# Kernel optimization log

Hardware: AMD Instinct MI355X
Metric: run time of the kernel (lower is better)

## Reference

```python
import jax, jax.numpy as jnp
import numpy as np

# MX microscaling decode helpers. Codes are stored as int32 holding uint8 bit patterns.
_FP4_MAG = jnp.array([0.0, 0.5, 1.0, 1.5, 2.0, 3.0, 4.0, 6.0], dtype=jnp.float32)  # E2M1

def dec_fp4(c):
    # c in [0,16): bit3 = sign, bits0-2 index E2M1 magnitude LUT
    s = jnp.where(c >= 8, -1.0, 1.0)
    return s * _FP4_MAG[c & 7]

def dec_fp6(c):
    # E3M2, bias 3. bit5 sign, bits2-4 exp, bits0-1 mantissa
    s = jnp.where(c >= 32, -1.0, 1.0)
    e = ((c >> 2) & 7).astype(jnp.float32)
    m = (c & 3).astype(jnp.float32)
    mag = jnp.where(e == 0, m * 0.25 * 0.25, (1.0 + m * 0.25) * jnp.exp2(e - 3.0))
    return s * mag

def dec_fp8(c):
    # E4M3, bias 7. bit7 sign, bits3-6 exp, bits0-2 mantissa (NaN code decoded as 480, consistent both sides)
    s = jnp.where(c >= 128, -1.0, 1.0)
    e = ((c >> 3) & 15).astype(jnp.float32)
    m = (c & 7).astype(jnp.float32)
    mag = jnp.where(e == 0, m * 0.125 * jnp.exp2(-6.0), (1.0 + m * 0.125) * jnp.exp2(e - 7.0))
    return s * mag

def unpack4(p):
    # [..., K//2] bytes -> [..., K] nibbles; low nibble = even element, high = odd
    lo = p & 15
    hi = (p >> 4) & 15
    return jnp.stack([lo, hi], axis=-1).reshape(*p.shape[:-1], p.shape[-1] * 2)

def unpack6(p):
    # little-endian 6-bit packing: 4 values per 3 bytes. [..., K*6//8] -> [..., K]
    g = p.reshape(*p.shape[:-1], -1, 3)
    b0, b1, b2 = g[..., 0], g[..., 1], g[..., 2]
    v0 = b0 & 0x3F
    v1 = ((b0 >> 6) & 3) | ((b1 & 0x0F) << 2)
    v2 = ((b1 >> 4) & 0x0F) | ((b2 & 3) << 4)
    v3 = (b2 >> 2) & 0x3F
    return jnp.stack([v0, v1, v2, v3], axis=-1).reshape(*p.shape[:-1], p.shape[-1] * 4 // 3)

def blockscale(x, sf):
    # x [..., K] fp32, sf [..., K//32] E8M0 exponents: scale = 2^(sf-127) per 32-element block
    scale = jnp.exp2(sf.astype(jnp.float32) - 127.0)
    xs = x.reshape(*x.shape[:-1], -1, 32) * scale[..., None]
    return xs.reshape(x.shape)

def dequant(codes, sf, bits):
    if bits == 4:
        x = dec_fp4(unpack4(codes))
    elif bits == 6:
        x = dec_fp6(unpack6(codes))
    else:
        x = dec_fp8(codes)
    return blockscale(x, sf)


def setup_inputs() -> dict:
    key = jax.random.key(0)
    ks = jax.random.split(key, 13)
    M, N = 4096, 4096
    p4, p6, p8 = 3072, 768, 256
    ri = lambda k, sh: jax.random.randint(k, sh, 0, 256, dtype=jnp.int32)
    sf = lambda k, sh: jax.random.randint(k, sh, 121, 132, dtype=jnp.int32)
    return {
        "AN": ri(ks[0], (M, p4 // 2)),
        "AS": ri(ks[1], (M, p6 * 6 // 8)),
        "AO": ri(ks[2], (M, p8)),
        "SFAN": sf(ks[3], (M, p4 // 32)),
        "SFAS": sf(ks[4], (M, p6 // 32)),
        "SFAO": sf(ks[5], (M, p8 // 32)),
        "BN": ri(ks[6], (N, p4 // 2)),
        "BS": ri(ks[7], (N, p6 * 6 // 8)),
        "BO": ri(ks[8], (N, p8)),
        "SFBN": sf(ks[9], (N * p4 // 32,)),
        "SFBS": sf(ks[10], (N * p6 // 32,)),
        "SFBO": sf(ks[11], (N * p8 // 32,)),
        "bias": jax.random.normal(ks[12], (N,), dtype=jnp.float32) * 0.02,
    }


def reference(AN, AS, AO, SFAN, SFAS, SFAO, BN, BS, BO, SFBN, SFBS, SFBO, bias):
    N = BN.shape[0]
    a4 = dequant(AN, SFAN, 4)                       # [M, p4]
    w4 = dequant(BN, SFBN.reshape(N, -1), 4)        # [N, p4]
    a6 = dequant(AS, SFAS, 6)                       # [M, p6]
    w6 = dequant(BS, SFBS.reshape(N, -1), 6)        # [N, p6]
    a8 = dequant(AO, SFAO, 8)                       # [M, p8]
    w8 = dequant(BO, SFBO.reshape(N, -1), 8)        # [N, p8]
    y = a4 @ w4.T + a6 @ w6.T + a8 @ w8.T           # [M, N]
    return y + bias
```

## Files before the change

kernel.cpp:

```cpp
#include <hip/hip_runtime.h>

typedef short short8 __attribute__((ext_vector_type(8)));
typedef int   intx8  __attribute__((ext_vector_type(8)));
typedef float floatx16 __attribute__((ext_vector_type(16)));

__device__ __forceinline__ unsigned pk4(int a, int b, int c, int d) {
    return (a & 255) | ((b & 255) << 8) | ((c & 255) << 16) | ((unsigned)(d & 255) << 24);
}

__device__ __forceinline__ unsigned dec8bf(int c, int esf) {
    int s = (c & 128) << 8;
    int e = (c >> 3) & 15, m = c & 7;
    int rn = s | ((e + 120 + esf) << 7) | (m << 4);
    int nb = (m >= 4) ? 2 : ((m >= 2) ? 1 : 0);
    int rs = m ? (s | ((nb + 118 + esf) << 7) | ((m << (7 - nb)) & 0x7F)) : s;
    return (unsigned)(e ? rn : rs);
}

__global__ __launch_bounds__(256) void pack_lds(
    const int* __restrict__ Pn, const int* __restrict__ Ps, const int* __restrict__ Po,
    const int* __restrict__ Sn, const int* __restrict__ Ss, const int* __restrict__ So,
    unsigned char* __restrict__ C4, unsigned char* __restrict__ C6,
    unsigned short* __restrict__ C8, unsigned char* __restrict__ St, int R)
{
    __shared__ unsigned lds[9216];
    int t = threadIdx.x, b = blockIdx.x, per = R >> 6;
    if (b < 4 * per) {
        int jg = b / per, rb = b - jg * per, r0 = rb << 6;
        #pragma unroll
        for (int i = 0; i < 24; ++i) {
            int idx = i * 256 + t, row = idx / 96, q4 = idx - row * 96;
            int4 v = *(const int4*)(Pn + (size_t)(r0 + row) * 1536 + jg * 384 + q4 * 4);
            lds[row * 96 + q4] = pk4(v.x, v.y, v.z, v.w);
        }
        __syncthreads();
        #pragma unroll
        for (int i = 0; i < 6; ++i) {
            int idx = i * 256 + t, j = idx >> 6, row = idx & 63;
            uint4 v = *(uint4*)&lds[row * 96 + j * 4];
            *(uint4*)(C4 + ((size_t)(jg * 24 + j) * R + r0 + row) * 16) = v;
        }
    } else if (b < 5 * per) {
        int rb = b - 4 * per, r0 = rb << 6;
        #pragma unroll
        for (int i = 0; i < 36; ++i) {
            int idx = i * 256 + t, row = idx / 144, q4 = idx - row * 144;
            int4 v = *(const int4*)(Ps + (size_t)(r0 + row) * 576 + q4 * 4);
            lds[row * 144 + q4] = pk4(v.x, v.y, v.z, v.w);
        }
        __syncthreads();
        #pragma unroll
        for (int i = 0; i < 18; ++i) {
            int idx = i * 256 + t, seg = idx / 192, off = idx - seg * 192;
            int row = off / 3, m3 = off - row * 3;
            int w0 = row * 144 + seg * 6 + m3 * 2;
            int2 v = { (int)lds[w0], (int)lds[w0 + 1] };
            *(int2*)(C6 + ((size_t)seg * R + r0) * 24 + (size_t)off * 8) = v;
        }
    } else if (b < 6 * per) {
        int rb = b - 5 * per, r0 = rb << 6;
        #pragma unroll
        for (int i = 0; i < 16; ++i) {
            int idx = i * 256 + t, row = idx >> 6, q4 = idx & 63;
            int4 c = *(const int4*)(Po + (size_t)(r0 + row) * 256 + q4 * 4);
            int e = So[(size_t)(r0 + row) * 8 + (q4 >> 3)] - 127;
            lds[row * 128 + q4 * 2]     = dec8bf(c.x & 255, e) | (dec8bf(c.y & 255, e) << 16);
            lds[row * 128 + q4 * 2 + 1] = dec8bf(c.z & 255, e) | (dec8bf(c.w & 255, e) << 16);
        }
        __syncthreads();
        #pragma unroll
        for (int i = 0; i < 8; ++i) {
            int idx = i * 256 + t, seg = idx >> 6, row = idx & 63;
            uint4 v = *(uint4*)&lds[row * 128 + seg * 4];
            *(uint4*)((unsigned char*)C8 + ((size_t)seg * R + r0 + row) * 16) = v;
        }
    } else if (b < 7 * per) {
        int rb = b - 6 * per, r0 = rb << 6;
        #pragma unroll
        for (int i = 0; i < 6; ++i) {
            int idx = i * 256 + t, row = idx / 24, q4 = idx - row * 24;
            int4 v = *(const int4*)(Sn + (size_t)(r0 + row) * 96 + q4 * 4);
            lds[row * 24 + q4] = pk4(v.x, v.y, v.z, v.w);
        }
        __syncthreads();
        #pragma unroll
        for (int i = 0; i < 6; ++i) {
            int idx = i * 256 + t, seg = idx >> 6, row = idx & 63;
            *(unsigned*)(St + ((size_t)seg * R + r0 + row) * 4) = lds[row * 24 + seg];
        }
    } else {
        int rb = b - 7 * per, r0 = rb << 6;
        #pragma unroll
        for (int i = 0; i < 3; ++i) {
            int idx = i * 256 + t, row = idx / 12, b2 = idx - row * 12;
            int2 v = *(const int2*)(Ss + (size_t)(r0 + row) * 24 + b2 * 2);
            lds[row * 12 + b2] = (unsigned)((v.x & 255) | ((v.y & 255) << 8));
        }
        __syncthreads();
        #pragma unroll
        for (int i = 0; i < 3; ++i) {
            int idx = i * 256 + t, seg = idx >> 6, row = idx & 63;
            *(unsigned*)(St + ((size_t)(24 + seg) * R + r0 + row) * 4) = lds[row * 12 + seg];
        }
    }
}

__global__ __launch_bounds__(256, 2) void gemm_mx(
    const unsigned char* __restrict__ A4, const unsigned char* __restrict__ B4,
    const unsigned char* __restrict__ A6, const unsigned char* __restrict__ B6,
    const unsigned short* __restrict__ A8, const unsigned short* __restrict__ B8,
    const unsigned char* __restrict__ SaT, const unsigned char* __restrict__ SbT,
    const float* __restrict__ bias, float* __restrict__ C, int M, int N)
{
    int tid = threadIdx.x, w = tid >> 6, l = tid & 63;
    int nbm = M >> 7, nbn = N >> 7;
    int bm, bn;
    if (nbm == 32 && nbn == 32) {
        int o = blockIdx.y * 32 + blockIdx.x;
        int xcd = o & 7, pos = o >> 3;
        int tile = pos >> 4, idx = pos & 15;
        bm = xcd * 4 + (idx & 3);
        bn = tile * 4 + (idx >> 2);
    } else { bm = blockIdx.y; bn = blockIdx.x; }

    int wm = (w >> 1) * 64, wn = (w & 1) * 64;
    int lr = l & 31, lh = l >> 5;

    floatx16 acc[2][2] = {};

    int rA[2] = { bm * 128 + wm + lr, bm * 128 + wm + 32 + lr };
    int cB[2] = { bn * 128 + wn + lr, bn * 128 + wn + 32 + lr };

    {
        unsigned strA = 32u * (unsigned)M, strB = 32u * (unsigned)N;
        unsigned fA0 = ((unsigned)lh * M + (unsigned)rA[0]) * 16u;
        unsigned fA1 = ((unsigned)lh * M + (unsigned)rA[1]) * 16u;
        unsigned fB0 = ((unsigned)lh * N + (unsigned)cB[0]) * 16u;
        unsigned fB1 = ((unsigned)lh * N + (unsigned)cB[1]) * 16u;

        int4 pa[4][2], pb[4][2];
        #pragma unroll
        for (int s = 0; s < 4; ++s) {
            pa[s][0] = *(const int4*)(A4 + fA0); pa[s][1] = *(const int4*)(A4 + fA1);
            pb[s][0] = *(const int4*)(B4 + fB0); pb[s][1] = *(const int4*)(B4 + fB1);
            fA0 += strA; fA1 += strA; fB0 += strB; fB1 += strB;
        }

        unsigned sstrA = 4u * (unsigned)M, sstrB = 4u * (unsigned)N;
        unsigned sA0 = (unsigned)rA[0] * 4u, sA1 = (unsigned)rA[1] * 4u;
        unsigned sB0 = (unsigned)cB[0] * 4u, sB1 = (unsigned)cB[1] * 4u;
        unsigned psa[2][2], psb[2][2];
        psa[0][0] = *(const unsigned*)(SaT + sA0);         psa[0][1] = *(const unsigned*)(SaT + sA1);
        psb[0][0] = *(const unsigned*)(SbT + sB0);         psb[0][1] = *(const unsigned*)(SbT + sB1);
        psa[1][0] = *(const unsigned*)(SaT + sA0 + sstrA); psa[1][1] = *(const unsigned*)(SaT + sA1 + sstrA);
        psb[1][0] = *(const unsigned*)(SbT + sB0 + sstrB); psb[1][1] = *(const unsigned*)(SbT + sB1 + sstrB);
        sA0 += 2 * sstrA; sA1 += 2 * sstrA; sB0 += 2 * sstrB; sB1 += 2 * sstrB;

        #pragma unroll 4
        for (int u = 0; u < 48; ++u) {
            int sl = u & 3, wsl = (u >> 1) & 1;
            int sh = 8 * ((u & 1) * 2 + lh);
            int sa0 = (int)((psa[wsl][0] >> sh) & 255), sa1 = (int)((psa[wsl][1] >> sh) & 255);
            int sb0 = (int)((psb[wsl][0] >> sh) & 255), sb1 = (int)((psb[wsl][1] >> sh) & 255);
            intx8 A0 = (intx8){ pa[sl][0].x, pa[sl][0].y, pa[sl][0].z, pa[sl][0].w, 0, 0, 0, 0 };
            intx8 A1 = (intx8){ pa[sl][1].x, pa[sl][1].y, pa[sl][1].z, pa[sl][1].w, 0, 0, 0, 0 };
            intx8 B0 = (intx8){ pb[sl][0].x, pb[sl][0].y, pb[sl][0].z, pb[sl][0].w, 0, 0, 0, 0 };
            intx8 B1 = (intx8){ pb[sl][1].x, pb[sl][1].y, pb[sl][1].z, pb[sl][1].w, 0, 0, 0, 0 };
            acc[0][0] = __builtin_amdgcn_mfma_scale_f32_32x32x64_f8f6f4(A0, B0, acc[0][0], 4, 4, 0, sa0, 0, sb0);
            acc[0][1] = __builtin_amdgcn_mfma_scale_f32_32x32x64_f8f6f4(A0, B1, acc[0][1], 4, 4, 0, sa0, 0, sb1);
            acc[1][0] = __builtin_amdgcn_mfma_scale_f32_32x32x64_f8f6f4(A1, B0, acc[1][0], 4, 4, 0, sa1, 0, sb0);
            acc[1][1] = __builtin_amdgcn_mfma_scale_f32_32x32x64_f8f6f4(A1, B1, acc[1][1], 4, 4, 0, sa1, 0, sb1);
            pa[sl][0] = *(const int4*)(A4 + fA0); pa[sl][1] = *(const int4*)(A4 + fA1);
            pb[sl][0] = *(const int4*)(B4 + fB0); pb[sl][1] = *(const int4*)(B4 + fB1);
            fA0 += strA; fA1 += strA; fB0 += strB; fB1 += strB;
            if (u & 1) {
                psa[wsl][0] = *(const unsigned*)(SaT + sA0); psa[wsl][1] = *(const unsigned*)(SaT + sA1);
                psb[wsl][0] = *(const unsigned*)(SbT + sB0); psb[wsl][1] = *(const unsigned*)(SbT + sB1);
                sA0 += sstrA; sA1 += sstrA; sB0 += sstrB; sB1 += sstrB;
            }
        }
    }

    {
        unsigned str6A = 48u * (unsigned)M, str6B = 48u * (unsigned)N;
        unsigned gA0 = ((unsigned)lh * M + (unsigned)rA[0]) * 24u;
        unsigned gA1 = ((unsigned)lh * M + (unsigned)rA[1]) * 24u;
        unsigned gB0 = ((unsigned)lh * N + (unsigned)cB[0]) * 24u;
        unsigned gB1 = ((unsigned)lh * N + (unsigned)cB[1]) * 24u;
        unsigned ss4A = 4u * (unsigned)M, ss4B = 4u * (unsigned)N;
        unsigned zA0 = (24u * (unsigned)M + (unsigned)rA[0]) * 4u;
        unsigned zA1 = (24u * (unsigned)M + (unsigned)rA[1]) * 4u;
        unsigned zB0 = (24u * (unsigned)N + (unsigned)cB[0]) * 4u;
        unsigned zB1 = (24u * (unsigned)N + (unsigned)cB[1]) * 4u;

        int2 qa[2][2][3], qb[2][2][3];
        unsigned p6a[2][2], p6b[2][2];
        #pragma unroll
        for (int s = 0; s < 2; ++s) {
            const unsigned char *a0 = A6 + gA0, *a1 = A6 + gA1, *b0 = B6 + gB0, *b1 = B6 + gB1;
            qa[s][0][0] = *(const int2*)(a0); qa[s][0][1] = *(const int2*)(a0 + 8); qa[s][0][2] = *(const int2*)(a0 + 16);
            qa[s][1][0] = *(const int2*)(a1); qa[s][1][1] = *(const int2*)(a1 + 8); qa[s][1][2] = *(const int2*)(a1 + 16);
            qb[s][0][0] = *(const int2*)(b0); qb[s][0][1] = *(const int2*)(b0 + 8); qb[s][0][2] = *(const int2*)(b0 + 16);
            qb[s][1][0] = *(const int2*)(b1); qb[s][1][1] = *(const int2*)(b1 + 8); qb[s][1][2] = *(const int2*)(b1 + 16);
            p6a[s][0] = *(const unsigned*)(SaT + zA0); p6a[s][1] = *(const unsigned*)(SaT + zA1);
            p6b[s][0] = *(const unsigned*)(SbT + zB0); p6b[s][1] = *(const unsigned*)(SbT + zB1);
            gA0 += str6A; gA1 += str6A; gB0 += str6B; gB1 += str6B;
            zA0 += ss4A; zA1 += ss4A; zB0 += ss4B; zB1 += ss4B;
        }
        int sh6 = 8 * lh;
        #pragma unroll 2
        for (int v = 0; v < 10; ++v) {
            int sl = v & 1;
            int sa0 = (int)((p6a[sl][0] >> sh6) & 255), sa1 = (int)((p6a[sl][1] >> sh6) & 255);
            int sb0 = (int)((p6b[sl][0] >> sh6) & 255), sb1 = (int)((p6b[sl][1] >> sh6) & 255);
            intx8 A0 = (intx8){ qa[sl][0][0].x, qa[sl][0][0].y, qa[sl][0][1].x, qa[sl][0][1].y, qa[sl][0][2].x, qa[sl][0][2].y, 0, 0 };
            intx8 A1 = (intx8){ qa[sl][1][0].x, qa[sl][1][0].y, qa[sl][1][1].x, qa[sl][1][1].y, qa[sl][1][2].x, qa[sl][1][2].y, 0, 0 };
            intx8 B0 = (intx8){ qb[sl][0][0].x, qb[sl][0][0].y, qb[sl][0][1].x, qb[sl][0][1].y, qb[sl][0][2].x, qb[sl][0][2].y, 0, 0 };
            intx8 B1 = (intx8){ qb[sl][1][0].x, qb[sl][1][0].y, qb[sl][1][1].x, qb[sl][1][1].y, qb[sl][1][2].x, qb[sl][1][2].y, 0, 0 };
            acc[0][0] = __builtin_amdgcn_mfma_scale_f32_32x32x64_f8f6f4(A0, B0, acc[0][0], 3, 3, 0, sa0, 0, sb0);
            acc[0][1] = __builtin_amdgcn_mfma_scale_f32_32x32x64_f8f6f4(A0, B1, acc[0][1], 3, 3, 0, sa0, 0, sb1);
            acc[1][0] = __builtin_amdgcn_mfma_scale_f32_32x32x64_f8f6f4(A1, B0, acc[1][0], 3, 3, 0, sa1, 0, sb0);
            acc[1][1] = __builtin_amdgcn_mfma_scale_f32_32x32x64_f8f6f4(A1, B1, acc[1][1], 3, 3, 0, sa1, 0, sb1);
            {
                const unsigned char *a0 = A6 + gA0, *a1 = A6 + gA1, *b0 = B6 + gB0, *b1 = B6 + gB1;
                qa[sl][0][0] = *(const int2*)(a0); qa[sl][0][1] = *(const int2*)(a0 + 8); qa[sl][0][2] = *(const int2*)(a0 + 16);
                qa[sl][1][0] = *(const int2*)(a1); qa[sl][1][1] = *(const int2*)(a1 + 8); qa[sl][1][2] = *(const int2*)(a1 + 16);
                qb[sl][0][0] = *(const int2*)(b0); qb[sl][0][1] = *(const int2*)(b0 + 8); qb[sl][0][2] = *(const int2*)(b0 + 16);
                qb[sl][1][0] = *(const int2*)(b1); qb[sl][1][1] = *(const int2*)(b1 + 8); qb[sl][1][2] = *(const int2*)(b1 + 16);
                p6a[sl][0] = *(const unsigned*)(SaT + zA0); p6a[sl][1] = *(const unsigned*)(SaT + zA1);
                p6b[sl][0] = *(const unsigned*)(SbT + zB0); p6b[sl][1] = *(const unsigned*)(SbT + zB1);
                gA0 += str6A; gA1 += str6A; gB0 += str6B; gB1 += str6B;
                zA0 += ss4A; zA1 += ss4A; zB0 += ss4B; zB1 += ss4B;
            }
        }
        #pragma unroll
        for (int v = 10; v < 12; ++v) {
            int sl = v & 1;
            int sa0 = (int)((p6a[sl][0] >> sh6) & 255), sa1 = (int)((p6a[sl][1] >> sh6) & 255);
            int sb0 = (int)((p6b[sl][0] >> sh6) & 255), sb1 = (int)((p6b[sl][1] >> sh6) & 255);
            intx8 A0 = (intx8){ qa[sl][0][0].x, qa[sl][0][0].y, qa[sl][0][1].x, qa[sl][0][1].y, qa[sl][0][2].x, qa[sl][0][2].y, 0, 0 };
            intx8 A1 = (intx8){ qa[sl][1][0].x, qa[sl][1][0].y, qa[sl][1][1].x, qa[sl][1][1].y, qa[sl][1][2].x, qa[sl][1][2].y, 0, 0 };
            intx8 B0 = (intx8){ qb[sl][0][0].x, qb[sl][0][0].y, qb[sl][0][1].x, qb[sl][0][1].y, qb[sl][0][2].x, qb[sl][0][2].y, 0, 0 };
            intx8 B1 = (intx8){ qb[sl][1][0].x, qb[sl][1][0].y, qb[sl][1][1].x, qb[sl][1][1].y, qb[sl][1][2].x, qb[sl][1][2].y, 0, 0 };
            acc[0][0] = __builtin_amdgcn_mfma_scale_f32_32x32x64_f8f6f4(A0, B0, acc[0][0], 3, 3, 0, sa0, 0, sb0);
            acc[0][1] = __builtin_amdgcn_mfma_scale_f32_32x32x64_f8f6f4(A0, B1, acc[0][1], 3, 3, 0, sa0, 0, sb1);
            acc[1][0] = __builtin_amdgcn_mfma_scale_f32_32x32x64_f8f6f4(A1, B0, acc[1][0], 3, 3, 0, sa1, 0, sb0);
            acc[1][1] = __builtin_amdgcn_mfma_scale_f32_32x32x64_f8f6f4(A1, B1, acc[1][1], 3, 3, 0, sa1, 0, sb1);
        }
    }

    {
        unsigned str8A = 32u * (unsigned)M, str8B = 32u * (unsigned)N;
        const unsigned char* A8b = (const unsigned char*)A8;
        const unsigned char* B8b = (const unsigned char*)B8;
        unsigned hA0 = ((unsigned)lh * M + (unsigned)rA[0]) * 16u;
        unsigned hA1 = ((unsigned)lh * M + (unsigned)rA[1]) * 16u;
        unsigned hB0 = ((unsigned)lh * N + (unsigned)cB[0]) * 16u;
        unsigned hB1 = ((unsigned)lh * N + (unsigned)cB[1]) * 16u;
        short8 ra[2][2], rb[2][2];
        #pragma unroll
        for (int s = 0; s < 2; ++s) {
            ra[s][0] = *(const short8*)(A8b + hA0); ra[s][1] = *(const short8*)(A8b + hA1);
            rb[s][0] = *(const short8*)(B8b + hB0); rb[s][1] = *(const short8*)(B8b + hB1);
            hA0 += str8A; hA1 += str8A; hB0 += str8B; hB1 += str8B;
        }
        #pragma unroll 2
        for (int q = 0; q < 16; ++q) {
            int sl = q & 1;
            acc[0][0] = __builtin_amdgcn_mfma_f32_32x32x16_bf16(ra[sl][0], rb[sl][0], acc[0][0], 0, 0, 0);
            acc[0][1] = __builtin_amdgcn_mfma_f32_32x32x16_bf16(ra[sl][0], rb[sl][1], acc[0][1], 0, 0, 0);
            acc[1][0] = __builtin_amdgcn_mfma_f32_32x32x16_bf16(ra[sl][1], rb[sl][0], acc[1][0], 0, 0, 0);
            acc[1][1] = __builtin_amdgcn_mfma_f32_32x32x16_bf16(ra[sl][1], rb[sl][1], acc[1][1], 0, 0, 0);
            ra[sl][0] = *(const short8*)(A8b + hA0); ra[sl][1] = *(const short8*)(A8b + hA1);
            rb[sl][0] = *(const short8*)(B8b + hB0); rb[sl][1] = *(const short8*)(B8b + hB1);
            hA0 += str8A; hA1 += str8A; hB0 += str8B; hB1 += str8B;
        }
    }

    #pragma unroll
    for (int i = 0; i < 2; i++)
        #pragma unroll
        for (int j = 0; j < 2; j++) {
            int col = bn * 128 + wn + j * 32 + lr;
            float bv = bias[col];
            #pragma unroll
            for (int r = 0; r < 16; r++) {
                int row = bm * 128 + wm + i * 32 + (r & 3) + 8 * (r >> 2) + 4 * lh;
                C[(size_t)row * N + col] = acc[i][j][r] + bv;
            }
        }
}

extern "C" void kernel_launch(void* const* d_in, const int* in_sizes, int n_in,
                              void* d_out, int out_size, void* d_ws, size_t ws_size,
                              hipStream_t stream) {
    const int* AN   = (const int*)d_in[0];
    const int* ASs  = (const int*)d_in[1];
    const int* AO   = (const int*)d_in[2];
    const int* SFAN = (const int*)d_in[3];
    const int* SFAS = (const int*)d_in[4];
    const int* SFAO = (const int*)d_in[5];
    const int* BN   = (const int*)d_in[6];
    const int* BS   = (const int*)d_in[7];
    const int* BO   = (const int*)d_in[8];
    const int* SFBN = (const int*)d_in[9];
    const int* SFBS = (const int*)d_in[10];
    const int* SFBO = (const int*)d_in[11];
    const float* bias = (const float*)d_in[12];

    int M = in_sizes[0] / 1536;
    int N = in_sizes[6] / 1536;

    unsigned char* ws = (unsigned char*)d_ws;
    size_t o = 0;
    unsigned char*  A4c = ws + o;                    o += (size_t)M * 1536;
    unsigned char*  B4c = ws + o;                    o += (size_t)N * 1536;
    unsigned char*  A6c = ws + o;                    o += (size_t)M * 576;
    unsigned char*  B6c = ws + o;                    o += (size_t)N * 576;
    unsigned short* A8d = (unsigned short*)(ws + o); o += (size_t)M * 512;
    unsigned short* B8d = (unsigned short*)(ws + o); o += (size_t)N * 512;
    unsigned char*  SaT = ws + o;                    o += (size_t)36 * M * 4;
    unsigned char*  SbT = ws + o;                    o += (size_t)36 * N * 4;

    pack_lds<<<(M >> 6) * 8, 256, 0, stream>>>(AN, ASs, AO, SFAN, SFAS, SFAO,
                                               A4c, A6c, A8d, SaT, M);
    pack_lds<<<(N >> 6) * 8, 256, 0, stream>>>(BN, BS, BO, SFBN, SFBS, SFBO,
                                               B4c, B6c, B8d, SbT, N);

    dim3 grid(N / 128, M / 128);
    gemm_mx<<<grid, 256, 0, stream>>>(A4c, B4c, A6c, B6c, A8d, B8d,
                                      SaT, SbT, bias, (float*)d_out, M, N);
}
```

Measured before the change: 220.1 us.

## Merge A/B pack launches, drop XCD swizzle, reorder loads before prioritized MFMAs

Merges the two pack launches into one kernel whose grid covers both A and B sides, saving a launch and letting the two halves overlap. In the GEMM main loops, the next-stage global loads are now issued before the MFMAs, and each MFMA group is wrapped in s_setprio raises to favour matrix issue. The XCD-aware block-to-tile remap is removed in favour of a plain blockIdx mapping, which may reduce L2 locality across XCDs.

```diff
diff --git a/kernel.cpp b/kernel.cpp
--- a/kernel.cpp
+++ b/kernel.cpp
@@ -17,14 +17,14 @@
     return (unsigned)(e ? rn : rs);
 }
 
-__global__ __launch_bounds__(256) void pack_lds(
+__device__ __forceinline__ void pack_side_lds(
+    int b, int t, unsigned* lds,
     const int* __restrict__ Pn, const int* __restrict__ Ps, const int* __restrict__ Po,
     const int* __restrict__ Sn, const int* __restrict__ Ss, const int* __restrict__ So,
     unsigned char* __restrict__ C4, unsigned char* __restrict__ C6,
     unsigned short* __restrict__ C8, unsigned char* __restrict__ St, int R)
 {
-    __shared__ unsigned lds[9216];
-    int t = threadIdx.x, b = blockIdx.x, per = R >> 6;
+    int per = R >> 6;
     if (b < 4 * per) {
         int jg = b / per, rb = b - jg * per, r0 = rb << 6;
         #pragma unroll
@@ -103,6 +103,23 @@
             *(unsigned*)(St + ((size_t)(24 + seg) * R + r0 + row) * 4) = lds[row * 12 + seg];
         }
     }
+}
+
+__global__ __launch_bounds__(256) void pack_all(
+    const int* __restrict__ AN, const int* __restrict__ AS, const int* __restrict__ AO,
+    const int* __restrict__ SAn, const int* __restrict__ SAs, const int* __restrict__ SAo,
+    unsigned char* __restrict__ A4, unsigned char* __restrict__ A6,
+    unsigned short* __restrict__ A8, unsigned char* __restrict__ SaT, int M,
+    const int* __restrict__ BN, const int* __restrict__ BS, const int* __restrict__ BO,
+    const int* __restrict__ SBn, const int* __restrict__ SBs, const int* __restrict__ SBo,
+    unsigned char* __restrict__ B4, unsigned char* __restrict__ B6,
+    unsigned short* __restrict__ B8, unsigned char* __restrict__ SbT, int N)
+{
+    __shared__ unsigned lds[9216];
+    int b = blockIdx.x, t = threadIdx.x;
+    int nA = (M >> 6) * 8;
+    if (b < nA) pack_side_lds(b, t, lds, AN, AS, AO, SAn, SAs, SAo, A4, A6, A8, SaT, M);
+    else        pack_side_lds(b - nA, t, lds, BN, BS, BO, SBn, SBs, SBo, B4, B6, B8, SbT, N);
 }
 
 __global__ __launch_bounds__(256, 2) void gemm_mx(
@@ -113,16 +130,7 @@
     const float* __restrict__ bias, float* __restrict__ C, int M, int N)
 {
     int tid = threadIdx.x, w = tid >> 6, l = tid & 63;
-    int nbm = M >> 7, nbn = N >> 7;
-    int bm, bn;
-    if (nbm == 32 && nbn == 32) {
-        int o = blockIdx.y * 32 + blockIdx.x;
-        int xcd = o & 7, pos = o >> 3;
-        int tile = pos >> 4, idx = pos & 15;
-        bm = xcd * 4 + (idx & 3);
-        bn = tile * 4 + (idx >> 2);
-    } else { bm = blockIdx.y; bn = blockIdx.x; }
-
+    int bm = blockIdx.y, bn = blockIdx.x;
     int wm = (w >> 1) * 64, wn = (w & 1) * 64;
     int lr = l & 31, lh = l >> 5;
 
@@ -159,17 +167,13 @@
         #pragma unroll 4
         for (int u = 0; u < 48; ++u) {
             int sl = u & 3, wsl = (u >> 1) & 1;
-            int sh = 8 * ((u & 1) * 2 + lh);
-            int sa0 = (int)((psa[wsl][0] >> sh) & 255), sa1 = (int)((psa[wsl][1] >> sh) & 255);
-            int sb0 = (int)((psb[wsl][0] >> sh) & 255), sb1 = (int)((psb[wsl][1] >> sh) & 255);
             intx8 A0 = (intx8){ pa[sl][0].x, pa[sl][0].y, pa[sl][0].z, pa[sl][0].w, 0, 0, 0, 0 };
             intx8 A1 = (intx8){ pa[sl][1].x, pa[sl][1].y, pa[sl][1].z, pa[sl][1].w, 0, 0, 0, 0 };
             intx8 B0 = (intx8){ pb[sl][0].x, pb[sl][0].y, pb[sl][0].z, pb[sl][0].w, 0, 0, 0, 0 };
             intx8 B1 = (intx8){ pb[sl][1].x, pb[sl][1].y, pb[sl][1].z, pb[sl][1].w, 0, 0, 0, 0 };
-            acc[0][0] = __builtin_amdgcn_mfma_scale_f32_32x32x64_f8f6f4(A0, B0, acc[0][0], 4, 4, 0, sa0, 0, sb0);
-            acc[0][1] = __builtin_amdgcn_mfma_scale_f32_32x32x64_f8f6f4(A0, B1, acc[0][1], 4, 4, 0, sa0, 0, sb1);
-            acc[1][0] = __builtin_amdgcn_mfma_scale_f32_32x32x64_f8f6f4(A1, B0, acc[1][0], 4, 4, 0, sa1, 0, sb0);
-            acc[1][1] = __builtin_amdgcn_mfma_scale_f32_32x32x64_f8f6f4(A1, B1, acc[1][1], 4, 4, 0, sa1, 0, sb1);
+            int sh = 8 * ((u & 1) * 2 + lh);
+            int sa0 = (int)((psa[wsl][0] >> sh) & 255), sa1 = (int)((psa[wsl][1] >> sh) & 255);
+            int sb0 = (int)((psb[wsl][0] >> sh) & 255), sb1 = (int)((psb[wsl][1] >> sh) & 255);
             pa[sl][0] = *(const int4*)(A4 + fA0); pa[sl][1] = *(const int4*)(A4 + fA1);
             pb[sl][0] = *(const int4*)(B4 + fB0); pb[sl][1] = *(const int4*)(B4 + fB1);
             fA0 += strA; fA1 += strA; fB0 += strB; fB1 += strB;
@@ -178,6 +182,12 @@
                 psb[wsl][0] = *(const unsigned*)(SbT + sB0); psb[wsl][1] = *(const unsigned*)(SbT + sB1);
                 sA0 += sstrA; sA1 += sstrA; sB0 += sstrB; sB1 += sstrB;
             }
+            __builtin_amdgcn_s_setprio(1);
+            acc[0][0] = __builtin_amdgcn_mfma_scale_f32_32x32x64_f8f6f4(A0, B0, acc[0][0], 4, 4, 0, sa0, 0, sb0);
+            acc[0][1] = __builtin_amdgcn_mfma_scale_f32_32x32x64_f8f6f4(A0, B1, acc[0][1], 4, 4, 0, sa0, 0, sb1);
+            acc[1][0] = __builtin_amdgcn_mfma_scale_f32_32x32x64_f8f6f4(A1, B0, acc[1][0], 4, 4, 0, sa1, 0, sb0);
+            acc[1][1] = __builtin_amdgcn_mfma_scale_f32_32x32x64_f8f6f4(A1, B1, acc[1][1], 4, 4, 0, sa1, 0, sb1);
+            __builtin_amdgcn_s_setprio(0);
         }
     }
 
@@ -217,10 +227,6 @@
             intx8 A1 = (intx8){ qa[sl][1][0].x, qa[sl][1][0].y, qa[sl][1][1].x, qa[sl][1][1].y, qa[sl][1][2].x, qa[sl][1][2].y, 0, 0 };
             intx8 B0 = (intx8){ qb[sl][0][0].x, qb[sl][0][0].y, qb[sl][0][1].x, qb[sl][0][1].y, qb[sl][0][2].x, qb[sl][0][2].y, 0, 0 };
             intx8 B1 = (intx8){ qb[sl][1][0].x, qb[sl][1][0].y, qb[sl][1][1].x, qb[sl][1][1].y, qb[sl][1][2].x, qb[sl][1][2].y, 0, 0 };
-            acc[0][0] = __builtin_amdgcn_mfma_scale_f32_32x32x64_f8f6f4(A0, B0, acc[0][0], 3, 3, 0, sa0, 0, sb0);
-            acc[0][1] = __builtin_amdgcn_mfma_scale_f32_32x32x64_f8f6f4(A0, B1, acc[0][1], 3, 3, 0, sa0, 0, sb1);
-            acc[1][0] = __builtin_amdgcn_mfma_scale_f32_32x32x64_f8f6f4(A1, B0, acc[1][0], 3, 3, 0, sa1, 0, sb0);
-            acc[1][1] = __builtin_amdgcn_mfma_scale_f32_32x32x64_f8f6f4(A1, B1, acc[1][1], 3, 3, 0, sa1, 0, sb1);
             {
                 const unsigned char *a0 = A6 + gA0, *a1 = A6 + gA1, *b0 = B6 + gB0, *b1 = B6 + gB1;
                 qa[sl][0][0] = *(const int2*)(a0); qa[sl][0][1] = *(const int2*)(a0 + 8); qa[sl][0][2] = *(const int2*)(a0 + 16);
@@ -232,6 +238,12 @@
                 gA0 += str6A; gA1 += str6A; gB0 += str6B; gB1 += str6B;
                 zA0 += ss4A; zA1 += ss4A; zB0 += ss4B; zB1 += ss4B;
             }
+            __builtin_amdgcn_s_setprio(1);
+            acc[0][0] = __builtin_amdgcn_mfma_scale_f32_32x32x64_f8f6f4(A0, B0, acc[0][0], 3, 3, 0, sa0, 0, sb0);
+            acc[0][1] = __builtin_amdgcn_mfma_scale_f32_32x32x64_f8f6f4(A0, B1, acc[0][1], 3, 3, 0, sa0, 0, sb1);
+            acc[1][0] = __builtin_amdgcn_mfma_scale_f32_32x32x64_f8f6f4(A1, B0, acc[1][0], 3, 3, 0, sa1, 0, sb0);
+            acc[1][1] = __builtin_amdgcn_mfma_scale_f32_32x32x64_f8f6f4(A1, B1, acc[1][1], 3, 3, 0, sa1, 0, sb1);
+            __builtin_amdgcn_s_setprio(0);
         }
         #pragma unroll
         for (int v = 10; v < 12; ++v) {
@@ -267,13 +279,16 @@
         #pragma unroll 2
         for (int q = 0; q < 16; ++q) {
             int sl = q & 1;
-            acc[0][0] = __builtin_amdgcn_mfma_f32_32x32x16_bf16(ra[sl][0], rb[sl][0], acc[0][0], 0, 0, 0);
-            acc[0][1] = __builtin_amdgcn_mfma_f32_32x32x16_bf16(ra[sl][0], rb[sl][1], acc[0][1], 0, 0, 0);
-            acc[1][0] = __builtin_amdgcn_mfma_f32_32x32x16_bf16(ra[sl][1], rb[sl][0], acc[1][0], 0, 0, 0);
-            acc[1][1] = __builtin_amdgcn_mfma_f32_32x32x16_bf16(ra[sl][1], rb[sl][1], acc[1][1], 0, 0, 0);
+            short8 a0 = ra[sl][0], a1 = ra[sl][1], b0 = rb[sl][0], b1 = rb[sl][1];
             ra[sl][0] = *(const short8*)(A8b + hA0); ra[sl][1] = *(const short8*)(A8b + hA1);
             rb[sl][0] = *(const short8*)(B8b + hB0); rb[sl][1] = *(const short8*)(B8b + hB1);
             hA0 += str8A; hA1 += str8A; hB0 += str8B; hB1 += str8B;
+            __builtin_amdgcn_s_setprio(1);
+            acc[0][0] = __builtin_amdgcn_mfma_f32_32x32x16_bf16(a0, b0, acc[0][0], 0, 0, 0);
+            acc[0][1] = __builtin_amdgcn_mfma_f32_32x32x16_bf16(a0, b1, acc[0][1], 0, 0, 0);
+            acc[1][0] = __builtin_amdgcn_mfma_f32_32x32x16_bf16(a1, b0, acc[1][0], 0, 0, 0);
+            acc[1][1] = __builtin_amdgcn_mfma_f32_32x32x16_bf16(a1, b1, acc[1][1], 0, 0, 0);
+            __builtin_amdgcn_s_setprio(0);
         }
     }
 
@@ -322,10 +337,10 @@
     unsigned char*  SaT = ws + o;                    o += (size_t)36 * M * 4;
     unsigned char*  SbT = ws + o;                    o += (size_t)36 * N * 4;
 
-    pack_lds<<<(M >> 6) * 8, 256, 0, stream>>>(AN, ASs, AO, SFAN, SFAS, SFAO,
-                                               A4c, A6c, A8d, SaT, M);
-    pack_lds<<<(N >> 6) * 8, 256, 0, stream>>>(BN, BS, BO, SFBN, SFBS, SFBO,
-                                               B4c, B6c, B8d, SbT, N);
+    int nblk = (M >> 6) * 8 + (N >> 6) * 8;
+    pack_all<<<nblk, 256, 0, stream>>>(
+        AN, ASs, AO, SFAN, SFAS, SFAO, A4c, A6c, A8d, SaT, M,
+        BN, BS, BO, SFBN, SFBS, SFBO, B4c, B6c, B8d, SbT, N);
 
     dim3 grid(N / 128, M / 128);
     gemm_mx<<<grid, 256, 0, stream>>>(A4c, B4c, A6c, B6c, A8d, B8d,
```

Measured after the change: 210.9 us. -4.2%, faster.
